# Optimization experiments

Hardware: AMD Instinct MI355X
Metric: run time of the kernel (lower is better)

The kernel has to match this reference:

```python
import jax, jax.numpy as jnp
import numpy as np

T, H, I, E, K = 4096, 1024, 768, 8, 2

def setup_inputs() -> dict:
    key = jax.random.key(0)
    k1, k2, k3, k4 = jax.random.split(key, 4)
    s_h = 1.0 / np.sqrt(H)
    s_i = 1.0 / np.sqrt(I)
    return {
        "hidden_states": jax.random.normal(k1, (T, H), dtype=jnp.float32),
        "gate_w": jax.random.normal(k2, (E, H), dtype=jnp.float32) * s_h,   # router, fp32
        "w13": jax.random.normal(k3, (E, 2 * I, H), dtype=jnp.float32) * s_h,  # fused gate+up
        "w2": jax.random.normal(k4, (E, H, I), dtype=jnp.float32) * s_i,
        "num_global_tokens": T,
        "max_num_tokens_per_gpu": T,
    }

def reference(hidden_states, gate_w, w13, w2, num_global_tokens, max_num_tokens_per_gpu):
    x = hidden_states  # [T, H]
    orig_dtype = x.dtype
    # router runs in fp32 (router_dtype == 'float32')
    router_logits = jnp.einsum('th,eh->te', x.astype(jnp.float32), gate_w)
    router_logits = router_logits.astype(orig_dtype)
    # FusedMoE top-k: softmax in fp32 over all experts, then top-k; renormalize=False
    probs = jax.nn.softmax(router_logits.astype(jnp.float32), axis=-1)  # [T, E]
    topk_w, topk_ids = jax.lax.top_k(probs, K)  # [T, K]
    # dense combine weights [T, E] (scatter of top-k weights)
    combine = jnp.sum(jax.nn.one_hot(topk_ids, E, dtype=topk_w.dtype) * topk_w[..., None], axis=1)
    combine = combine.astype(orig_dtype)
    # dense per-expert SwiGLU MLP, masked-combined (grouped GEMM reference)
    h = jnp.einsum('th,ejh->tej', x, w13)  # [T, E, 2I]
    g, u = h[..., :I], h[..., I:]
    a = jax.nn.silu(g) * u                 # [T, E, I]
    o = jnp.einsum('tei,ehi->teh', a, w2)  # [T, E, H]
    out = jnp.einsum('teh,te->th', o, combine)  # routed_scaling_factor = 1.0
    return out.reshape(x.shape)
```

## Files before the change

### kernel.cpp

```cpp
#include <hip/hip_runtime.h>
#include <hip/hip_bf16.h>

#define TT 4096
#define HH 1024
#define II 768
#define EE 8
#define TWOI 1536
#define MAXT 72

typedef __attribute__((ext_vector_type(8))) short bf16x8;
typedef __attribute__((ext_vector_type(4))) float f32x4;

__device__ unsigned short g_x_bf[TT * HH];
__device__ unsigned short g_w13_bf[EE * TWOI * HH];
__device__ unsigned short g_w2_bf[EE * HH * II];
__device__ unsigned short g_a[EE * TT * II];
__device__ float g_opart[2 * TT * HH];
__device__ int g_perm_tok[EE * TT];
__device__ float g_perm_w[EE * TT];
__device__ int g_perm_slot[EE * TT];
__device__ int g_cnt[EE];
__device__ int g_e1[TT];
__device__ int g_e2[TT];
__device__ float g_w1f[TT];
__device__ float g_w2f[TT];
__device__ int g_tile_e[MAXT];
__device__ int g_tile_row[MAXT];
__device__ int g_ntiles;

__device__ __forceinline__ unsigned short f2bf(float f) {
  union { float f; unsigned u; } v; v.f = f;
  unsigned r = v.u + 0x7fff + ((v.u >> 16) & 1);
  return (unsigned short)(r >> 16);
}

__device__ __forceinline__ void gload16(const void* g, void* l) {
  __builtin_amdgcn_global_load_lds(
      (const __attribute__((address_space(1))) void*)g,
      (__attribute__((address_space(3))) void*)l, 16, 0, 0);
}

__device__ __forceinline__ void cvt_chunks(const float* __restrict__ in,
                                           unsigned short* __restrict__ dst,
                                           int nKB, int chunk) {
  const int lane = threadIdx.x & 63;
  const int r16 = lane & 15, c8 = lane >> 4;
  const int jbg = chunk / nKB, kb = chunk - jbg * nKB;
  const float* src = in + ((size_t)jbg * 16 + r16) * ((size_t)nKB * 32) + kb * 32 + c8 * 8;
  float4 v0 = *(const float4*)(src);
  float4 v1 = *(const float4*)(src + 4);
  ushort4 o0, o1;
  o0.x = f2bf(v0.x); o0.y = f2bf(v0.y); o0.z = f2bf(v0.z); o0.w = f2bf(v0.w);
  o1.x = f2bf(v1.x); o1.y = f2bf(v1.y); o1.z = f2bf(v1.z); o1.w = f2bf(v1.w);
  unsigned short* d = dst + (size_t)chunk * 512 + lane * 8;
  *(ushort4*)(d) = o0;
  *(ushort4*)(d + 4) = o1;
}

__global__ __launch_bounds__(256) void k_prep(const float* __restrict__ x,
                                              const float* __restrict__ gw,
                                              const float* __restrict__ w13,
                                              const float* __restrict__ w2) {
  const int b = blockIdx.x;
  const int wv = threadIdx.x >> 6;
  if (b >= 1024) {
    if (b < 7168) cvt_chunks(w13, g_w13_bf, 32, (b - 1024) * 4 + wv);
    else          cvt_chunks(w2,  g_w2_bf,  24, (b - 7168) * 4 + wv);
    return;
  }
  const int lane = threadIdx.x & 63;
  const int t = b * 4 + wv;

  const float* xr = x + (size_t)t * HH + lane * 16;
  float4 xv0 = *(const float4*)(xr + 0);
  float4 xv1 = *(const float4*)(xr + 4);
  float4 xv2 = *(const float4*)(xr + 8);
  float4 xv3 = *(const float4*)(xr + 12);

  unsigned short* xd = g_x_bf + (size_t)t * HH + lane * 16;
  ushort4 o0, o1, o2, o3;
  o0.x = f2bf(xv0.x); o0.y = f2bf(xv0.y); o0.z = f2bf(xv0.z); o0.w = f2bf(xv0.w);
  o1.x = f2bf(xv1.x); o1.y = f2bf(xv1.y); o1.z = f2bf(xv1.z); o1.w = f2bf(xv1.w);
  o2.x = f2bf(xv2.x); o2.y = f2bf(xv2.y); o2.z = f2bf(xv2.z); o2.w = f2bf(xv2.w);
  o3.x = f2bf(xv3.x); o3.y = f2bf(xv3.y); o3.z = f2bf(xv3.z); o3.w = f2bf(xv3.w);
  *(ushort4*)(xd + 0) = o0;
  *(ushort4*)(xd + 4) = o1;
  *(ushort4*)(xd + 8) = o2;
  *(ushort4*)(xd + 12) = o3;

  float lg[EE];
#pragma unroll
  for (int ei = 0; ei < EE; ++ei) {
    const float* gr = gw + ei * HH + lane * 16;
    float4 g0 = *(const float4*)(gr + 0);
    float4 g1 = *(const float4*)(gr + 4);
    float4 g2 = *(const float4*)(gr + 8);
    float4 g3 = *(const float4*)(gr + 12);
    float a = xv0.x * g0.x + xv0.y * g0.y + xv0.z * g0.z + xv0.w * g0.w
            + xv1.x * g1.x + xv1.y * g1.y + xv1.z * g1.z + xv1.w * g1.w
            + xv2.x * g2.x + xv2.y * g2.y + xv2.z * g2.z + xv2.w * g2.w
            + xv3.x * g3.x + xv3.y * g3.y + xv3.z * g3.z + xv3.w * g3.w;
#pragma unroll
    for (int s = 32; s > 0; s >>= 1) a += __shfl_xor(a, s);
    lg[ei] = a;
  }

  if (lane == 0) {
    float mx = lg[0];
#pragma unroll
    for (int ei = 1; ei < EE; ++ei) mx = fmaxf(mx, lg[ei]);
    float p[EE]; float s = 0.f;
#pragma unroll
    for (int ei = 0; ei < EE; ++ei) { p[ei] = expf(lg[ei] - mx); s += p[ei]; }
    float inv = 1.f / s;
    int e1 = 0; float b1 = lg[0];
#pragma unroll
    for (int ei = 1; ei < EE; ++ei) if (lg[ei] > b1) { b1 = lg[ei]; e1 = ei; }
    int e2 = -1; float b2 = -3.0e38f;
#pragma unroll
    for (int ei = 0; ei < EE; ++ei)
      if (ei != e1 && lg[ei] > b2) { b2 = lg[ei]; e2 = ei; }

    g_e1[t] = e1;
    g_e2[t] = e2;
    g_w1f[t] = p[e1] * inv;
    g_w2f[t] = p[e2] * inv;
  }
}

__global__ __launch_bounds__(256) void k_route2() {
  const int e = blockIdx.x;
  const int tid = threadIdx.x;
  __shared__ int pre[256];

  const int t0 = tid * (TT / 256);
  int c = 0;
#pragma unroll
  for (int j = 0; j < TT / 256; ++j) {
    int t = t0 + j;
    if (g_e1[t] == e) ++c;
    if (g_e2[t] == e) ++c;
  }
  pre[tid] = c;
  __syncthreads();
  for (int off = 1; off < 256; off <<= 1) {
    int v = (tid >= off) ? pre[tid - off] : 0;
    __syncthreads();
    pre[tid] += v;
    __syncthreads();
  }
  int pos = pre[tid] - c;
#pragma unroll
  for (int j = 0; j < TT / 256; ++j) {
    int t = t0 + j;
    if (g_e1[t] == e) {
      g_perm_tok[e * TT + pos] = t;
      g_perm_w[e * TT + pos] = g_w1f[t];
      g_perm_slot[e * TT + pos] = 0;
      ++pos;
    }
    if (g_e2[t] == e) {
      g_perm_tok[e * TT + pos] = t;
      g_perm_w[e * TT + pos] = g_w2f[t];
      g_perm_slot[e * TT + pos] = 1;
      ++pos;
    }
  }
  if (tid == 255) g_cnt[e] = pre[255];
}

__global__ void k_prefix() {
  if (threadIdx.x == 0) {
    int t = 0;
    for (int e = 0; e < EE; ++e) {
      int c = g_cnt[e];
      for (int rb = 0; rb < c; rb += 128) {
        g_tile_e[t] = e;
        g_tile_row[t] = rb;
        ++t;
      }
    }
    g_ntiles = t;
  }
}

__global__ __launch_bounds__(512) void k_gemm1() {
  const int bid = blockIdx.x;
  const int xcd = bid & 7;
  const int k = bid >> 3;
  const int tile = xcd + 8 * (k / 6);
  const int cb = k % 6;
  if (tile >= g_ntiles) return;
  const int e = g_tile_e[tile];
  const int rowbase = g_tile_row[tile];
  const int cnt = g_cnt[e];
  const int tid = threadIdx.x;
  const int lane = tid & 63;
  const int wid = tid >> 6;
  const int wm = wid >> 1;
  const int wc = wid & 1;

  __shared__ uint4 sA[3][512];
  __shared__ uint4 sBg[3][512];
  __shared__ uint4 sBu[3][512];

  const int r16 = lane & 15;
  const int c8 = lane >> 4;
  const int arow = rowbase + wid * 16 + r16;
  const int tok = (arow < cnt) ? g_perm_tok[e * TT + arow] : 0;
  const unsigned short* aptr = g_x_bf + (size_t)tok * HH + c8 * 8;
  const unsigned short* bgp =
      g_w13_bf + ((size_t)(e * 96 + cb * 8 + wid) * 32) * 512 + lane * 8;
  const unsigned short* bup = bgp + (size_t)48 * 32 * 512;

  const int soff = __builtin_amdgcn_readfirstlane(wid * 1024);

#define STG1(buf, kk) do { \
    gload16(aptr + (kk) * 32, (char*)sA + (buf) * 8192 + soff); \
    gload16(bgp + (size_t)(kk) * 512, (char*)sBg + (buf) * 8192 + soff); \
    gload16(bup + (size_t)(kk) * 512, (char*)sBu + (buf) * 8192 + soff); \
  } while (0)

  f32x4 accg[2][4], accu[2][4];
#pragma unroll
  for (int m = 0; m < 2; ++m)
#pragma unroll
    for (int n = 0; n < 4; ++n) {
      accg[m][n] = (f32x4){0.f, 0.f, 0.f, 0.f};
      accu[m][n] = (f32x4){0.f, 0.f, 0.f, 0.f};
    }

  STG1(0, 0);
  STG1(1, 1);
  for (int ks = 0; ks < 32; ++ks) {
    const int cur = ks % 3;
    if (ks < 30) {
      const int stg = (ks + 2) % 3;
      STG1(stg, ks + 2);
      asm volatile("s_waitcnt vmcnt(6)" ::: "memory");
    } else if (ks == 30) {
      asm volatile("s_waitcnt vmcnt(3)" ::: "memory");
    } else {
      asm volatile("s_waitcnt vmcnt(0)" ::: "memory");
    }
    __builtin_amdgcn_s_barrier();
    __builtin_amdgcn_sched_barrier(0);
    bf16x8 af[2], bgf[4], buf_[4];
#pragma unroll
    for (int m = 0; m < 2; ++m)
      af[m] = *(const bf16x8*)((const char*)sA + cur * 8192 + (wm * 2 + m) * 1024 + lane * 16);
#pragma unroll
    for (int n = 0; n < 4; ++n) {
      int jb = wc * 4 + n;
      bgf[n] = *(const bf16x8*)((const char*)sBg + cur * 8192 + jb * 1024 + lane * 16);
      buf_[n] = *(const bf16x8*)((const char*)sBu + cur * 8192 + jb * 1024 + lane * 16);
    }
#pragma unroll
    for (int m = 0; m < 2; ++m)
#pragma unroll
      for (int n = 0; n < 4; ++n) {
        accg[m][n] = __builtin_amdgcn_mfma_f32_16x16x32_bf16(af[m], bgf[n], accg[m][n], 0, 0, 0);
        accu[m][n] = __builtin_amdgcn_mfma_f32_16x16x32_bf16(af[m], buf_[n], accu[m][n], 0, 0, 0);
      }
    __builtin_amdgcn_sched_barrier(0);
    __builtin_amdgcn_s_barrier();
  }
#undef STG1

  const int rhi = lane >> 4, clo = lane & 15;
  unsigned short* abase = g_a + ((size_t)(e * 256 + (rowbase >> 4)) * 24) * 512;
#pragma unroll
  for (int m = 0; m < 2; ++m) {
#pragma unroll
    for (int jj = 0; jj < 4; ++jj) {
      int rbl = wm * 2 + m;
      int rr = rhi * 4 + jj;
      int row = rowbase + rbl * 16 + rr;
      if (row < cnt) {
#pragma unroll
        for (int n = 0; n < 4; ++n) {
          int kb = cb * 4 + wc * 2 + (n >> 1);
          int sub = (2 * n + (clo >> 3)) & 3;
          float gv = accg[m][n][jj];
          float uv = accu[m][n][jj];
          float av = gv / (1.f + __expf(-gv)) * uv;
          abase[((size_t)rbl * 24 + kb) * 512 + sub * 128 + rr * 8 + (clo & 7)] = f2bf(av);
        }
      }
    }
  }
}

__global__ __launch_bounds__(512) void k_gemm2() {
  const int bid = blockIdx.x;
  const int xcd = bid & 7;
  const int k = bid >> 3;
  const int tile = xcd + 8 * (k >> 3);
  const int cb = k & 7;
  if (tile >= g_ntiles) return;
  const int e = g_tile_e[tile];
  const int rowbase = g_tile_row[tile];
  const int cnt = g_cnt[e];
  const int tid = threadIdx.x;
  const int lane = tid & 63;
  const int wid = tid >> 6;
  const int wm = wid >> 1;
  const int wc = wid & 1;

  __shared__ uint4 sA[3][512];
  __shared__ uint4 sB[3][512];
  __shared__ int s_tok[128];
  __shared__ float s_w[128];
  __shared__ int s_slot[128];

  if (tid < 128) {
    int row = rowbase + tid;
    bool v = row < cnt;
    s_tok[tid] = v ? g_perm_tok[e * TT + row] : 0;
    s_w[tid] = v ? g_perm_w[e * TT + row] : 0.f;
    s_slot[tid] = v ? g_perm_slot[e * TT + row] : 0;
  }

  const unsigned short* aptr =
      g_a + ((size_t)(e * 256 + (rowbase >> 4) + wid) * 24) * 512 + lane * 8;
  const unsigned short* bp =
      g_w2_bf + ((size_t)(e * 64 + cb * 8 + wid) * 24) * 512 + lane * 8;

  const int soff = __builtin_amdgcn_readfirstlane(wid * 1024);

#define STG2(buf, kk) do { \
    gload16(aptr + (size_t)(kk) * 512, (char*)sA + (buf) * 8192 + soff); \
    gload16(bp + (size_t)(kk) * 512, (char*)sB + (buf) * 8192 + soff); \
  } while (0)

  f32x4 acc[2][4];
#pragma unroll
  for (int m = 0; m < 2; ++m)
#pragma unroll
    for (int n = 0; n < 4; ++n) acc[m][n] = (f32x4){0.f, 0.f, 0.f, 0.f};

  STG2(0, 0);
  STG2(1, 1);
  for (int ks = 0; ks < 24; ++ks) {
    const int cur = ks % 3;
    if (ks < 22) {
      const int stg = (ks + 2) % 3;
      STG2(stg, ks + 2);
      asm volatile("s_waitcnt vmcnt(4)" ::: "memory");
    } else if (ks == 22) {
      asm volatile("s_waitcnt vmcnt(2)" ::: "memory");
    } else {
      asm volatile("s_waitcnt vmcnt(0)" ::: "memory");
    }
    __builtin_amdgcn_s_barrier();
    __builtin_amdgcn_sched_barrier(0);
    bf16x8 af[2], bfr[4];
#pragma unroll
    for (int m = 0; m < 2; ++m)
      af[m] = *(const bf16x8*)((const char*)sA + cur * 8192 + (wm * 2 + m) * 1024 + lane * 16);
#pragma unroll
    for (int n = 0; n < 4; ++n)
      bfr[n] = *(const bf16x8*)((const char*)sB + cur * 8192 + (wc * 4 + n) * 1024 + lane * 16);
#pragma unroll
    for (int m = 0; m < 2; ++m)
#pragma unroll
      for (int n = 0; n < 4; ++n)
        acc[m][n] = __builtin_amdgcn_mfma_f32_16x16x32_bf16(af[m], bfr[n], acc[m][n], 0, 0, 0);
    __builtin_amdgcn_sched_barrier(0);
    __builtin_amdgcn_s_barrier();
  }
#undef STG2

  const int rhi = lane >> 4, clo = lane & 15;
#pragma unroll
  for (int m = 0; m < 2; ++m) {
#pragma unroll
    for (int jj = 0; jj < 4; ++jj) {
      int rloc = wm * 32 + m * 16 + rhi * 4 + jj;
      if (rowbase + rloc < cnt) {
        int tok = s_tok[rloc];
        float w = s_w[rloc];
        float* orow = g_opart + (size_t)s_slot[rloc] * TT * HH + (size_t)tok * HH;
#pragma unroll
        for (int n = 0; n < 4; ++n) {
          int h2 = cb * 128 + wc * 64 + n * 16 + clo;
          orow[h2] = w * acc[m][n][jj];
        }
      }
    }
  }
}

__global__ __launch_bounds__(256) void k_combine(float* __restrict__ out) {
  int idx = (blockIdx.x * 256 + threadIdx.x) * 4;
  float4 p0 = *(const float4*)(g_opart + idx);
  float4 p1 = *(const float4*)(g_opart + TT * HH + idx);
  float4 o;
  o.x = p0.x + p1.x; o.y = p0.y + p1.y; o.z = p0.z + p1.z; o.w = p0.w + p1.w;
  *(float4*)(out + idx) = o;
}

extern "C" void kernel_launch(void* const* d_in, const int* in_sizes, int n_in,
                              void* d_out, int out_size, void* d_ws, size_t ws_size,
                              hipStream_t stream) {
  (void)in_sizes; (void)n_in; (void)d_ws; (void)ws_size; (void)out_size;
  const float* x   = (const float*)d_in[0];
  const float* gw  = (const float*)d_in[1];
  const float* w13 = (const float*)d_in[2];
  const float* w2  = (const float*)d_in[3];
  float* out = (float*)d_out;

  k_prep<<<dim3(10240), dim3(256), 0, stream>>>(x, gw, w13, w2);
  k_route2<<<dim3(EE), dim3(256), 0, stream>>>();
  k_prefix<<<dim3(1), dim3(64), 0, stream>>>();
  k_gemm1<<<dim3(MAXT * 6), dim3(512), 0, stream>>>();
  k_gemm2<<<dim3(MAXT * 8), dim3(512), 0, stream>>>();
  k_combine<<<dim3(TT * HH / 1024), dim3(256), 0, stream>>>(out);
}
```

Measured before the change: 127.6 us.

## Drop tile-prefix kernel, use fixed per-expert tile grid, overlap w2 conversion with GEMM1

Removes the single-thread k_prefix kernel and its tile tables. Both GEMM kernels now derive expert and row base straight from the block index, with a fixed capacity of ten 128-row tiles per expert, and exit early when a tile is past the expert's token count. The w2 fp32→bf16 conversion moves out of k_prep into extra blocks of the k_gemm1 launch, so it runs alongside the first GEMM. This saves a launch and the serial prefix step, and it pins each expert to one XCD via bid&7. In exchange, any expert receiving more than 1280 tokens would silently lose rows.

```diff
diff --git a/kernel.cpp b/kernel.cpp
--- a/kernel.cpp
+++ b/kernel.cpp
@@ -6,7 +6,6 @@
 #define II 768
 #define EE 8
 #define TWOI 1536
-#define MAXT 72
 
 typedef __attribute__((ext_vector_type(8))) short bf16x8;
 typedef __attribute__((ext_vector_type(4))) float f32x4;
@@ -24,9 +23,6 @@
 __device__ int g_e2[TT];
 __device__ float g_w1f[TT];
 __device__ float g_w2f[TT];
-__device__ int g_tile_e[MAXT];
-__device__ int g_tile_row[MAXT];
-__device__ int g_ntiles;
 
 __device__ __forceinline__ unsigned short f2bf(float f) {
   union { float f; unsigned u; } v; v.f = f;
@@ -59,13 +55,11 @@
 
 __global__ __launch_bounds__(256) void k_prep(const float* __restrict__ x,
                                               const float* __restrict__ gw,
-                                              const float* __restrict__ w13,
-                                              const float* __restrict__ w2) {
+                                              const float* __restrict__ w13) {
   const int b = blockIdx.x;
   const int wv = threadIdx.x >> 6;
   if (b >= 1024) {
-    if (b < 7168) cvt_chunks(w13, g_w13_bf, 32, (b - 1024) * 4 + wv);
-    else          cvt_chunks(w2,  g_w2_bf,  24, (b - 7168) * 4 + wv);
+    cvt_chunks(w13, g_w13_bf, 32, (b - 1024) * 4 + wv);
     return;
   }
   const int lane = threadIdx.x & 63;
@@ -169,34 +163,21 @@
   if (tid == 255) g_cnt[e] = pre[255];
 }
 
-__global__ void k_prefix() {
-  if (threadIdx.x == 0) {
-    int t = 0;
-    for (int e = 0; e < EE; ++e) {
-      int c = g_cnt[e];
-      for (int rb = 0; rb < c; rb += 128) {
-        g_tile_e[t] = e;
-        g_tile_row[t] = rb;
-        ++t;
-      }
-    }
-    g_ntiles = t;
-  }
-}
-
-__global__ __launch_bounds__(512) void k_gemm1() {
+__global__ __launch_bounds__(512) void k_gemm1(const float* __restrict__ w2) {
   const int bid = blockIdx.x;
-  const int xcd = bid & 7;
+  const int lane = threadIdx.x & 63;
+  const int wid = threadIdx.x >> 6;
+  if (bid >= 480) {
+    int chunk = (bid - 480) * 8 + wid;
+    if (chunk < EE * 64 * 24) cvt_chunks(w2, g_w2_bf, 24, chunk);
+    return;
+  }
+  const int e = bid & 7;
   const int k = bid >> 3;
-  const int tile = xcd + 8 * (k / 6);
   const int cb = k % 6;
-  if (tile >= g_ntiles) return;
-  const int e = g_tile_e[tile];
-  const int rowbase = g_tile_row[tile];
+  const int rowbase = (k / 6) * 128;
   const int cnt = g_cnt[e];
-  const int tid = threadIdx.x;
-  const int lane = tid & 63;
-  const int wid = tid >> 6;
+  if (rowbase >= cnt) return;
   const int wm = wid >> 1;
   const int wc = wid & 1;
 
@@ -293,14 +274,12 @@
 
 __global__ __launch_bounds__(512) void k_gemm2() {
   const int bid = blockIdx.x;
-  const int xcd = bid & 7;
+  const int e = bid & 7;
   const int k = bid >> 3;
-  const int tile = xcd + 8 * (k >> 3);
-  const int cb = k & 7;
-  if (tile >= g_ntiles) return;
-  const int e = g_tile_e[tile];
-  const int rowbase = g_tile_row[tile];
+  const int cb = k % 8;
+  const int rowbase = (k / 8) * 128;
   const int cnt = g_cnt[e];
+  if (rowbase >= cnt) return;
   const int tid = threadIdx.x;
   const int lane = tid & 63;
   const int wid = tid >> 6;
@@ -410,10 +389,9 @@
   const float* w2  = (const float*)d_in[3];
   float* out = (float*)d_out;
 
-  k_prep<<<dim3(10240), dim3(256), 0, stream>>>(x, gw, w13, w2);
+  k_prep<<<dim3(7168), dim3(256), 0, stream>>>(x, gw, w13);
   k_route2<<<dim3(EE), dim3(256), 0, stream>>>();
-  k_prefix<<<dim3(1), dim3(64), 0, stream>>>();
-  k_gemm1<<<dim3(MAXT * 6), dim3(512), 0, stream>>>();
-  k_gemm2<<<dim3(MAXT * 8), dim3(512), 0, stream>>>();
+  k_gemm1<<<dim3(480 + 1536), dim3(512), 0, stream>>>(w2);
+  k_gemm2<<<dim3(640), dim3(512), 0, stream>>>();
   k_combine<<<dim3(TT * HH / 1024), dim3(256), 0, stream>>>(out);
 }
```

New measurement: 116.0 us. -9.1%, faster.
